# Optimization experiments

Hardware: AMD Instinct MI355X
Metric: run time of the kernel (lower is better)

Reference implementation:

```python
import jax, jax.numpy as jnp
import numpy as np

N, K, P, A, NBINS, RP = 4096, 48, 128, 5, 16, 32
LN_EPS = 1e-5

def _normalize(v, eps=1e-6):
    return v / jnp.sqrt(jnp.maximum((v * v).sum(-1, keepdims=True), eps))

def extract_frames(pos):
    # pos: [N, A, 3]; atom order N, CA, C, ... -> Gram-Schmidt backbone frame
    n, ca, c = pos[:, 0], pos[:, 1], pos[:, 2]
    e1 = _normalize(c - ca)
    v2 = n - ca
    e2 = _normalize(v2 - (v2 * e1).sum(-1, keepdims=True) * e1)
    e3 = jnp.cross(e1, e2)
    R = jnp.stack([e1, e2, e3], axis=-1)  # [N,3,3], columns = frame axes
    return R, ca

def distance_rbf(d, d_min=0.0, d_max=22.0, bins=NBINS):
    step = (d_max - d_min) / bins
    centers = d_min + step * jnp.arange(bins, dtype=d.dtype)
    return jnp.exp(-(((d[..., None] - centers) / step) ** 2))

def relpos_features(resi, chain, batch, neighbours):
    # clipped relative sequence position, extra class for cross-chain/batch pairs
    rel = jnp.clip(resi[neighbours] - resi[:, None], -RP, RP) + RP
    same = (chain[neighbours] == chain[:, None]) & (batch[neighbours] == batch[:, None])
    cls = jnp.where(same, rel, 2 * RP + 1)
    return jax.nn.one_hot(cls, 2 * RP + 2, dtype=jnp.float32)  # [N,K,66]

def distance_features(pos, neighbours):
    pn = pos[neighbours]  # [N,K,A,3] gather
    diff = pos[:, None, :, None] - pn[:, :, None, :]  # [N,K,A,A,3]
    d = jnp.sqrt(jnp.maximum((diff * diff).sum(-1), 1e-12))
    return distance_rbf(d).reshape(N, K, A * A * NBINS)

def direction_features(pos, neighbours, R, ca):
    rel = pos[neighbours] - ca[:, None, None]  # [N,K,A,3]
    local = jnp.einsum('nji,nkaj->nkai', R, rel)  # express in frame of residue i
    return _normalize(local).reshape(N, K, A * 3)

def rotation_features(neighbours, R):
    Rrel = jnp.einsum('nji,nkjl->nkil', R, R[neighbours])  # R_i^T R_j
    return Rrel.reshape(N, K, 9)

def pair_vector_features(pos, neighbours, R, ca):
    rel = pos[neighbours] - ca[:, None, None]
    local = jnp.einsum('nji,nkaj->nkai', R, rel)
    return local.reshape(N, K, A * 3)

def setup_inputs() -> dict:
    key = jax.random.key(0)
    ks = jax.random.split(key, 12)
    s = 0.02
    pos = 5.0 * jax.random.normal(ks[0], (N, A, 3), dtype=jnp.float32)
    dmap = 22.0 * jax.random.uniform(ks[1], (N, N), dtype=jnp.float32)
    mask = jnp.ones((N,), dtype=jnp.float32)
    neighbours = jax.random.randint(ks[2], (N, K), 0, N, dtype=jnp.int32)
    resi = jnp.arange(N, dtype=jnp.int32)
    chain = jnp.zeros((N,), dtype=jnp.int32)
    batch = jnp.zeros((N,), dtype=jnp.int32)
    W_relpos = s * jax.random.normal(ks[3], (2 * RP + 2, P), dtype=jnp.float32)
    W_dmap = s * jax.random.normal(ks[4], (NBINS, P), dtype=jnp.float32)
    W_dist = s * jax.random.normal(ks[5], (A * A * NBINS, P), dtype=jnp.float32)
    W_dir = s * jax.random.normal(ks[6], (3 * A, P), dtype=jnp.float32)
    W_rot = s * jax.random.normal(ks[7], (9, P), dtype=jnp.float32)
    W_vec = s * jax.random.normal(ks[8], (3 * A, P), dtype=jnp.float32)
    ln_scale = jnp.ones((P,), dtype=jnp.float32)
    ln_offset = jnp.zeros((P,), dtype=jnp.float32)
    W1 = s * jax.random.normal(ks[9], (P, 2 * P), dtype=jnp.float32)
    b1 = jnp.zeros((2 * P,), dtype=jnp.float32)
    W2 = s * jax.random.normal(ks[10], (2 * P, P), dtype=jnp.float32)
    b2 = jnp.zeros((P,), dtype=jnp.float32)
    return dict(pos=pos, dmap=dmap, mask=mask, W_relpos=W_relpos, W_dmap=W_dmap,
                W_dist=W_dist, W_dir=W_dir, W_rot=W_rot, W_vec=W_vec,
                ln_scale=ln_scale, ln_offset=ln_offset, W1=W1, b1=b1, W2=W2, b2=b2,
                neighbours=neighbours, resi=resi, chain=chain, batch=batch)

def reference(pos, dmap, mask, W_relpos, W_dmap, W_dist, W_dir, W_rot, W_vec,
              ln_scale, ln_offset, W1, b1, W2, b2, neighbours, resi, chain, batch):
    pair_mask = mask[:, None] * mask[neighbours] * (neighbours != -1).astype(mask.dtype)
    R, ca = extract_frames(pos)
    idx = jnp.arange(N)
    dmap_nb = dmap[idx[:, None], neighbours]  # [N,K] gather of distance map
    # multi-branch linear sum
    pair = relpos_features(resi, chain, batch, neighbours) @ W_relpos
    pair += jnp.where(pair_mask[..., None] > 0, distance_rbf(dmap_nb), 0.0) @ W_dmap
    pair += distance_features(pos, neighbours) @ W_dist
    pair += direction_features(pos, neighbours, R, ca) @ W_dir
    pair += rotation_features(neighbours, R) @ W_rot
    pair += pair_vector_features(pos, neighbours, R, ca) @ W_vec
    # LayerNorm (create_scale=True, create_offset=True)
    mu = pair.mean(-1, keepdims=True)
    var = ((pair - mu) ** 2).mean(-1, keepdims=True)
    pair = (pair - mu) / jnp.sqrt(var + LN_EPS) * ln_scale + ln_offset
    # MLP(2P -> P) with gelu
    pair = jax.nn.gelu(pair @ W1 + b1) @ W2 + b2
    return pair, pair_mask
```

## Files before the change

### kernel.cpp

```cpp
#include <hip/hip_runtime.h>
#include <hip/hip_bf16.h>

#define N_RES 4096
#define KNB   48
#define PCH   128
#define INV_STEP 0.727272727272727f
#define E2INV 0.13533528323661270f

typedef __bf16 bf16x8 __attribute__((ext_vector_type(8)));
typedef float  f32x4  __attribute__((ext_vector_type(4)));

#define FOCT(o,m) (((o)*49 + (m))*8)

__device__ __align__(16) unsigned short g_wcat[60*128*8];
__device__ __align__(16) unsigned short g_w1[16*256*8];
__device__ __align__(16) unsigned short g_w2[32*128*8];

__device__ __forceinline__ unsigned short f2bf(float f) {
  unsigned int u = __float_as_uint(f);
  return (unsigned short)((u + 0x7fffu + ((u >> 16) & 1u)) >> 16);
}
__device__ __forceinline__ unsigned int pk2(float a, float b) {
  __hip_bfloat162 h = __float22bfloat162_rn(make_float2(a, b));
  unsigned int u; __builtin_memcpy(&u, &h, 4); return u;
}
__device__ __forceinline__ float gelu_f(float x) {
  float p = x * x;
  float q = fmaf(p, 0.044715f, 1.0f);
  float r = x * q;
  float e = __expf(-1.5957691216057308f * r);
  return x * __builtin_amdgcn_rcpf(1.0f + e);
}
__device__ __forceinline__ void frame_from_pos(const float* p, float* R) {
  float cax = p[3], cay = p[4], caz = p[5];
  float e1x = p[6]-cax, e1y = p[7]-cay, e1z = p[8]-caz;
  float i1 = __builtin_amdgcn_rsqf(fmaxf(e1x*e1x + e1y*e1y + e1z*e1z, 1e-6f));
  e1x *= i1; e1y *= i1; e1z *= i1;
  float vx = p[0]-cax, vy = p[1]-cay, vz = p[2]-caz;
  float dp = vx*e1x + vy*e1y + vz*e1z;
  float e2x = vx - dp*e1x, e2y = vy - dp*e1y, e2z = vz - dp*e1z;
  float i2 = __builtin_amdgcn_rsqf(fmaxf(e2x*e2x + e2y*e2y + e2z*e2z, 1e-6f));
  e2x *= i2; e2y *= i2; e2z *= i2;
  float e3x = e1y*e2z - e1z*e2y;
  float e3y = e1z*e2x - e1x*e2z;
  float e3z = e1x*e2y - e1y*e2x;
  R[0]=e1x; R[1]=e2x; R[2]=e3x;
  R[3]=e1y; R[4]=e2y; R[5]=e3y;
  R[6]=e1z; R[7]=e2z; R[8]=e3z;
}

__device__ __forceinline__ void stage_bins(unsigned short* sF, const float* s_xall,
                                           int xbase, int ntasks, int t) {
  for (int i = t; i < ntasks; i += 256) {
    int rloc = i / 48;
    int m = i - 48*rloc;
    float x = fminf(s_xall[(xbase + rloc)*48 + m], 25.0f);
    float u  = __expf(-x*x);
    float wu = __expf(2.0f*x - 1.0f);
    float xm = x - 15.0f;
    float d  = __expf(-xm*xm);
    float wd = __expf(-2.0f*xm - 1.0f);
    float bins[16];
    bins[0] = u;
    #pragma unroll
    for (int b = 1; b < 16; ++b) { u *= wu; wu *= E2INV; bins[b] = u; }
    bins[15] = fmaxf(bins[15], d);
    #pragma unroll
    for (int b = 14; b >= 0; --b) { d *= wd; wd *= E2INV; bins[b] = fmaxf(bins[b], d); }
    unsigned int p0 = pk2(bins[0], bins[1]),  p1 = pk2(bins[2], bins[3]);
    unsigned int p2 = pk2(bins[4], bins[5]),  p3 = pk2(bins[6], bins[7]);
    unsigned int p4 = pk2(bins[8], bins[9]),  p5 = pk2(bins[10], bins[11]);
    unsigned int p6 = pk2(bins[12], bins[13]),p7 = pk2(bins[14], bins[15]);
    int base = FOCT(2*rloc, m);
    *(uint4*)(sF + base)       = make_uint4(p0,p1,p2,p3);
    *(uint4*)(sF + base + 392) = make_uint4(p4,p5,p6,p7);
  }
}

__global__ __launch_bounds__(256) void prep_weights(
    const float* __restrict__ W_dmap, const float* __restrict__ W_dist,
    const float* __restrict__ W_dir, const float* __restrict__ W_rot,
    const float* __restrict__ W_vec, const float* __restrict__ W1,
    const float* __restrict__ W2)
{
  int i = blockIdx.x*256 + threadIdx.x;
  unsigned short pk[8];
  if (i < 7680) {
    int oct = i >> 7, col = i & 127;
    #pragma unroll
    for (int j = 0; j < 8; ++j) {
      int k = oct*8 + j;
      float v;
      if      (k < 16)  v = W_dmap[k*128 + col];
      else if (k < 416) v = W_dist[(k-16)*128 + col];
      else if (k < 456) {
        int a = (k-416) >> 3, jj = (k-416) & 7;
        v = (jj < 3) ? W_dir[(a*3+jj)*128 + col]
          : (jj < 6) ? W_vec[(a*3+jj-3)*128 + col] : 0.0f;
      }
      else if (k < 465) v = W_rot[(k-456)*128 + col];
      else              v = 0.0f;
      pk[j] = f2bf(v);
    }
    *(uint4*)(g_wcat + i*8) = *(uint4*)pk;
  } else if (i < 11776) {
    int j2 = i - 7680;
    int oct = j2 >> 8, col = j2 & 255;
    #pragma unroll
    for (int j = 0; j < 8; ++j) {
      int k = oct*8 + j;
      int h = 32*(k>>5) + (k&1)*16 + ((k&31)>>1);
      pk[j] = f2bf(W1[h*256 + col]);
    }
    *(uint4*)(g_w1 + j2*8) = *(uint4*)pk;
  } else if (i < 15872) {
    int j3 = i - 11776;
    int oct = j3 >> 7, col = j3 & 127;
    #pragma unroll
    for (int j = 0; j < 8; ++j) {
      int k = oct*8 + j;
      int kh = k & 127;
      int h = (k>>7)*128 + 32*(kh>>5) + (kh&1)*16 + ((kh&31)>>1);
      pk[j] = f2bf(W2[h*128 + col]);
    }
    *(uint4*)(g_w2 + j3*8) = *(uint4*)pk;
  }
}

#define MFMA6(A0,A1,A2,B0,B1,ACC) \
  ACC[0][0] = __builtin_amdgcn_mfma_f32_16x16x32_bf16(A0, B0, ACC[0][0], 0,0,0); \
  ACC[1][0] = __builtin_amdgcn_mfma_f32_16x16x32_bf16(A1, B0, ACC[1][0], 0,0,0); \
  ACC[2][0] = __builtin_amdgcn_mfma_f32_16x16x32_bf16(A2, B0, ACC[2][0], 0,0,0); \
  ACC[0][1] = __builtin_amdgcn_mfma_f32_16x16x32_bf16(A0, B1, ACC[0][1], 0,0,0); \
  ACC[1][1] = __builtin_amdgcn_mfma_f32_16x16x32_bf16(A1, B1, ACC[1][1], 0,0,0); \
  ACC[2][1] = __builtin_amdgcn_mfma_f32_16x16x32_bf16(A2, B1, ACC[2][1], 0,0,0);

__global__ __launch_bounds__(256, 6) void fused_struct_kernel(
    const float* __restrict__ pos, const float* __restrict__ dmap,
    const float* __restrict__ mask, const float* __restrict__ W_relpos,
    const float* __restrict__ ln_scale, const float* __restrict__ ln_offset,
    const float* __restrict__ b1, const float* __restrict__ b2,
    const int* __restrict__ neighbours, const int* __restrict__ resi,
    const int* __restrict__ chain, const int* __restrict__ batch,
    float* __restrict__ out)
{
  const int n = blockIdx.x;
  const int t = threadIdx.x;
  const int lane = t & 63;
  const int wv   = t >> 6;
  const int ln15 = lane & 15;
  const int quad = lane >> 4;

  __shared__ __align__(16) char regF[12544];
  __shared__ __align__(16) char regP[12544];
  __shared__ __align__(16) float2 s_stats[48];

  unsigned short* sF    = (unsigned short*)regF;
  unsigned short* sPair = (unsigned short*)regP;
  float*  s_posnb = (float*)regP;
  float*  s_Rnb   = (float*)(regP + 3264);
  float*  s_xall  = (float*)(regP + 5760);
  float*  s_posn  = (float*)(regP + 10752);
  float*  s_Rn    = (float*)(regP + 10816);
  int*    s_cls   = (int*)  (regP + 10880);
  float2* s_part  = (float2*)(regP + 11072);

  if (t < KNB) {
    const int k = t;
    const int nbraw = neighbours[n*KNB + k];
    int nb = nbraw; if (nb < 0) nb += N_RES;
    float p[15];
    const float* pp = pos + nb*15;
    #pragma unroll
    for (int d = 0; d < 15; ++d) { p[d] = pp[d]; s_posnb[k*17+d] = p[d]; }
    float R[9];
    frame_from_pos(p, R);
    #pragma unroll
    for (int d = 0; d < 9; ++d) s_Rnb[k*13+d] = R[d];

    float pm = mask[n] * mask[nb] * ((nbraw != -1) ? 1.0f : 0.0f);
    out[N_RES*KNB*PCH + n*KNB + k] = pm;

    int rel = resi[nb] - resi[n];
    rel = (rel < -32) ? -32 : (rel > 32 ? 32 : rel);
    rel += 32;
    bool same = (chain[nb] == chain[n]) && (batch[nb] == batch[n]);
    s_cls[k] = same ? rel : 65;

    float xd = dmap[(long long)n*N_RES + nb] * INV_STEP;
    s_xall[k] = (pm > 0.0f) ? xd : 30.0f;
  } else if (t == 255) {
    float p[15];
    const float* pp = pos + n*15;
    #pragma unroll
    for (int d = 0; d < 15; ++d) { p[d] = pp[d]; s_posn[d] = p[d]; }
    float R[9];
    frame_from_pos(p, R);
    #pragma unroll
    for (int d = 0; d < 9; ++d) s_Rn[d] = R[d];
  }
  __syncthreads();

  for (int idx = t; idx < 1200; idx += 256) {
    int c = idx / 48, k = idx - 48*c;
    int a1 = c / 5, a2 = c - 5*a1;
    float dx = s_posn[a1*3+0] - s_posnb[k*17 + a2*3+0];
    float dy = s_posn[a1*3+1] - s_posnb[k*17 + a2*3+1];
    float dz = s_posn[a1*3+2] - s_posnb[k*17 + a2*3+2];
    float d2 = dx*dx + dy*dy + dz*dz;
    s_xall[48 + idx] = sqrtf(fmaxf(d2, 1e-12f)) * INV_STEP;
  }

  float rp0[12], rp1[12];
  {
    int c0 = 32*wv + ln15;
    #pragma unroll
    for (int mt = 0; mt < 3; ++mt)
      #pragma unroll
      for (int r = 0; r < 4; ++r) {
        int row = mt*16 + quad*4 + r;
        const float* wr = W_relpos + s_cls[row]*128 + c0;
        rp0[mt*4+r] = wr[0];
        rp1[mt*4+r] = wr[16];
      }
  }
  __syncthreads();

  f32x4 acc1[3][2] = {};

  #pragma unroll 1
  for (int st = 0; st < 3; ++st) {
    stage_bins(sF, s_xall, st*8, 384, t);
    __syncthreads();
    #pragma unroll
    for (int kc = 0; kc < 4; ++kc) {
      const unsigned short* ab = sF + FOCT(kc*4 + quad, ln15);
      bf16x8 a0 = *(const bf16x8*)(ab);
      bf16x8 a1 = *(const bf16x8*)(ab + 128);
      bf16x8 a2 = *(const bf16x8*)(ab + 256);
      const unsigned short* bb = g_wcat + (((st*4+kc)*4 + quad)*128 + 32*wv + ln15)*8;
      bf16x8 b0 = *(const bf16x8*)(bb);
      bf16x8 b1v= *(const bf16x8*)(bb + 128);
      MFMA6(a0,a1,a2,b0,b1v,acc1)
    }
    __syncthreads();
  }

  stage_bins(sF, s_xall, 24, 96, t);
  if (t < 240) {
    int k = t / 5, a = t - 5*k;
    float rx = s_posnb[k*17 + a*3+0] - s_posn[3];
    float ry = s_posnb[k*17 + a*3+1] - s_posn[4];
    float rz = s_posnb[k*17 + a*3+2] - s_posn[5];
    float l0 = s_Rn[0]*rx + s_Rn[3]*ry + s_Rn[6]*rz;
    float l1 = s_Rn[1]*rx + s_Rn[4]*ry + s_Rn[7]*rz;
    float l2 = s_Rn[2]*rx + s_Rn[5]*ry + s_Rn[8]*rz;
    float inv = __builtin_amdgcn_rsqf(fmaxf(l0*l0 + l1*l1 + l2*l2, 1e-6f));
    *(uint4*)(sF + FOCT(4+a, k)) =
        make_uint4(pk2(l0*inv, l1*inv), pk2(l2*inv, l0), pk2(l1, l2), 0u);
  }
  if (t >= 208) {
    int k = t - 208;
    float rr[9];
    #pragma unroll
    for (int il = 0; il < 9; ++il) {
      int i2 = il / 3, l2c = il - 3*i2;
      rr[il] = s_Rn[0+i2]*s_Rnb[k*13 + 0+l2c]
             + s_Rn[3+i2]*s_Rnb[k*13 + 3+l2c]
             + s_Rn[6+i2]*s_Rnb[k*13 + 6+l2c];
    }
    *(uint4*)(sF + FOCT(9, k))  = make_uint4(pk2(rr[0],rr[1]), pk2(rr[2],rr[3]),
                                             pk2(rr[4],rr[5]), pk2(rr[6],rr[7]));
    *(uint4*)(sF + FOCT(10, k)) = make_uint4(pk2(rr[8],0.0f), 0u, 0u, 0u);
    *(uint4*)(sF + FOCT(11, k)) = make_uint4(0u, 0u, 0u, 0u);
  }
  __syncthreads();
  #pragma unroll
  for (int kc = 0; kc < 3; ++kc) {
    const unsigned short* ab = sF + FOCT(kc*4 + quad, ln15);
    bf16x8 a0 = *(const bf16x8*)(ab);
    bf16x8 a1 = *(const bf16x8*)(ab + 128);
    bf16x8 a2 = *(const bf16x8*)(ab + 256);
    const unsigned short* bb = g_wcat + (((12+kc)*4 + quad)*128 + 32*wv + ln15)*8;
    bf16x8 b0 = *(const bf16x8*)(bb);
    bf16x8 b1v= *(const bf16x8*)(bb + 128);
    MFMA6(a0,a1,a2,b0,b1v,acc1)
  }

  #pragma unroll
  for (int mt = 0; mt < 3; ++mt)
    #pragma unroll
    for (int r = 0; r < 4; ++r) {
      acc1[mt][0][r] += rp0[mt*4+r];
      acc1[mt][1][r] += rp1[mt*4+r];
    }

  #pragma unroll
  for (int mt = 0; mt < 3; ++mt)
    #pragma unroll
    for (int r = 0; r < 4; ++r) {
      float a0v = acc1[mt][0][r], a1v = acc1[mt][1][r];
      float sv = a0v + a1v;
      float qv = a0v*a0v + a1v*a1v;
      #pragma unroll
      for (int msk = 1; msk < 16; msk <<= 1) {
        sv += __shfl_xor(sv, msk);
        qv += __shfl_xor(qv, msk);
      }
      if (ln15 == 0) s_part[wv*48 + mt*16 + quad*4 + r] = make_float2(sv, qv);
    }
  __syncthreads();
  if (t < 48) {
    float S = 0.0f, Q = 0.0f;
    #pragma unroll
    for (int w = 0; w < 4; ++w) { float2 p = s_part[w*48 + t]; S += p.x; Q += p.y; }
    float mu = S * (1.0f/128.0f);
    float var = Q * (1.0f/128.0f) - mu*mu;
    s_stats[t] = make_float2(mu, __builtin_amdgcn_rsqf(var + 1e-5f));
  }
  __syncthreads();
  {
    int c0 = 32*wv + ln15;
    float gg0 = ln_scale[c0],  gg1 = ln_scale[c0+16];
    float oo0 = ln_offset[c0], oo1 = ln_offset[c0+16];
    int kp = 32*wv + 2*ln15;
    int oct = kp >> 3, slot = kp & 7;
    #pragma unroll
    for (int mt = 0; mt < 3; ++mt)
      #pragma unroll
      for (int r = 0; r < 4; ++r) {
        int row = mt*16 + quad*4 + r;
        float2 stt = s_stats[row];
        float v0 = (acc1[mt][0][r] - stt.x)*stt.y*gg0 + oo0;
        float v1 = (acc1[mt][1][r] - stt.x)*stt.y*gg1 + oo1;
        *(unsigned int*)(sPair + FOCT(oct,row) + slot) = pk2(v0, v1);
      }
  }
  __syncthreads();

  f32x4 acc3[3][2] = {};
  #pragma unroll 1
  for (int half = 0; half < 2; ++half) {
    f32x4 acc2[3][2] = {};
    #pragma unroll
    for (int kc = 0; kc < 4; ++kc) {
      const unsigned short* ab = sPair + FOCT(kc*4 + quad, ln15);
      bf16x8 a0 = *(const bf16x8*)(ab);
      bf16x8 a1 = *(const bf16x8*)(ab + 128);
      bf16x8 a2 = *(const bf16x8*)(ab + 256);
      const unsigned short* bb = g_w1 + ((kc*4 + quad)*256 + half*128 + 32*wv + ln15)*8;
      bf16x8 b0 = *(const bf16x8*)(bb);
      bf16x8 b1v= *(const bf16x8*)(bb + 128);
      MFMA6(a0,a1,a2,b0,b1v,acc2)
    }
    __syncthreads();
    {
      int hc = half*128 + 32*wv + ln15;
      float bb0 = b1[hc], bb1 = b1[hc+16];
      int kp = 32*wv + 2*ln15;
      int oct = kp >> 3, slot = kp & 7;
      #pragma unroll
      for (int mt = 0; mt < 3; ++mt)
        #pragma unroll
        for (int r = 0; r < 4; ++r) {
          int row = mt*16 + quad*4 + r;
          float h0 = gelu_f(acc2[mt][0][r] + bb0);
          float h1 = gelu_f(acc2[mt][1][r] + bb1);
          *(unsigned int*)(sF + FOCT(oct,row) + slot) = pk2(h0, h1);
        }
    }
    __syncthreads();
    #pragma unroll
    for (int kc = 0; kc < 4; ++kc) {
      const unsigned short* ab = sF + FOCT(kc*4 + quad, ln15);
      bf16x8 a0 = *(const bf16x8*)(ab);
      bf16x8 a1 = *(const bf16x8*)(ab + 128);
      bf16x8 a2 = *(const bf16x8*)(ab + 256);
      const unsigned short* bb = g_w2 + (((half*4 + kc)*4 + quad)*128 + 32*wv + ln15)*8;
      bf16x8 b0 = *(const bf16x8*)(bb);
      bf16x8 b1v= *(const bf16x8*)(bb + 128);
      MFMA6(a0,a1,a2,b0,b1v,acc3)
    }
  }

  {
    int c0 = 32*wv + ln15;
    float bo0 = b2[c0], bo1 = b2[c0+16];
    #pragma unroll
    for (int mt = 0; mt < 3; ++mt)
      #pragma unroll
      for (int r = 0; r < 4; ++r) {
        int row = mt*16 + quad*4 + r;
        out[(n*KNB + row)*PCH + c0]      = acc3[mt][0][r] + bo0;
        out[(n*KNB + row)*PCH + c0 + 16] = acc3[mt][1][r] + bo1;
      }
  }
}

extern "C" void kernel_launch(void* const* d_in, const int* in_sizes, int n_in,
                              void* d_out, int out_size, void* d_ws, size_t ws_size,
                              hipStream_t stream) {
  const float* pos       = (const float*)d_in[0];
  const float* dmap      = (const float*)d_in[1];
  const float* mask      = (const float*)d_in[2];
  const float* W_relpos  = (const float*)d_in[3];
  const float* W_dmap    = (const float*)d_in[4];
  const float* W_dist    = (const float*)d_in[5];
  const float* W_dir     = (const float*)d_in[6];
  const float* W_rot     = (const float*)d_in[7];
  const float* W_vec     = (const float*)d_in[8];
  const float* ln_scale  = (const float*)d_in[9];
  const float* ln_offset = (const float*)d_in[10];
  const float* W1        = (const float*)d_in[11];
  const float* b1        = (const float*)d_in[12];
  const float* W2        = (const float*)d_in[13];
  const float* b2        = (const float*)d_in[14];
  const int* neighbours  = (const int*)d_in[15];
  const int* resi        = (const int*)d_in[16];
  const int* chain       = (const int*)d_in[17];
  const int* batch       = (const int*)d_in[18];
  float* out = (float*)d_out;

  hipLaunchKernelGGL(prep_weights, dim3(62), dim3(256), 0, stream,
                     W_dmap, W_dist, W_dir, W_rot, W_vec, W1, W2);
  hipLaunchKernelGGL(fused_struct_kernel, dim3(N_RES), dim3(256), 0, stream,
                     pos, dmap, mask, W_relpos, ln_scale, ln_offset, b1, b2,
                     neighbours, resi, chain, batch, out);
}
```

Measured before the change: 293.7 us.

## Compute both MLP hidden halves at once and defer relpos weight gather

The two-pass loop over the MLP hidden dimension is replaced by one pass that computes all 256 hidden columns together. The GELU output goes to two shared buffers (sF and the reused pair buffer), and the second matmul then runs as a single 8-chunk loop. This removes two barriers and the serialized half loop, and lets more MFMAs issue back to back. The relpos weight gather now happens after the first GEMM instead of being held in 24 registers across it. The price is more live accumulator registers, which could raise register pressure or cause spills under launch_bounds(256,6), and the regP buffer grows slightly.

```diff
diff --git a/kernel.cpp b/kernel.cpp
--- a/kernel.cpp
+++ b/kernel.cpp
@@ -152,7 +152,7 @@
   const int quad = lane >> 4;
 
   __shared__ __align__(16) char regF[12544];
-  __shared__ __align__(16) char regP[12544];
+  __shared__ __align__(16) char regP[12672];
   __shared__ __align__(16) float2 s_stats[48];
 
   unsigned short* sF    = (unsigned short*)regF;
@@ -209,20 +209,6 @@
     float dz = s_posn[a1*3+2] - s_posnb[k*17 + a2*3+2];
     float d2 = dx*dx + dy*dy + dz*dz;
     s_xall[48 + idx] = sqrtf(fmaxf(d2, 1e-12f)) * INV_STEP;
-  }
-
-  float rp0[12], rp1[12];
-  {
-    int c0 = 32*wv + ln15;
-    #pragma unroll
-    for (int mt = 0; mt < 3; ++mt)
-      #pragma unroll
-      for (int r = 0; r < 4; ++r) {
-        int row = mt*16 + quad*4 + r;
-        const float* wr = W_relpos + s_cls[row]*128 + c0;
-        rp0[mt*4+r] = wr[0];
-        rp1[mt*4+r] = wr[16];
-      }
   }
   __syncthreads();
 
@@ -287,13 +273,18 @@
     MFMA6(a0,a1,a2,b0,b1v,acc1)
   }
 
-  #pragma unroll
-  for (int mt = 0; mt < 3; ++mt)
-    #pragma unroll
-    for (int r = 0; r < 4; ++r) {
-      acc1[mt][0][r] += rp0[mt*4+r];
-      acc1[mt][1][r] += rp1[mt*4+r];
-    }
+  {
+    int c0 = 32*wv + ln15;
+    #pragma unroll
+    for (int mt = 0; mt < 3; ++mt)
+      #pragma unroll
+      for (int r = 0; r < 4; ++r) {
+        int row = mt*16 + quad*4 + r;
+        const float* wr = W_relpos + s_cls[row]*128 + c0;
+        acc1[mt][0][r] += wr[0];
+        acc1[mt][1][r] += wr[16];
+      }
+  }
 
   #pragma unroll
   for (int mt = 0; mt < 3; ++mt)
@@ -338,49 +329,53 @@
   }
   __syncthreads();
 
+  f32x4 acc2a[3][2] = {};
+  f32x4 acc2b[3][2] = {};
+  #pragma unroll
+  for (int kc = 0; kc < 4; ++kc) {
+    const unsigned short* ab = sPair + FOCT(kc*4 + quad, ln15);
+    bf16x8 a0 = *(const bf16x8*)(ab);
+    bf16x8 a1 = *(const bf16x8*)(ab + 128);
+    bf16x8 a2 = *(const bf16x8*)(ab + 256);
+    const unsigned short* bb = g_w1 + ((kc*4 + quad)*256 + 32*wv + ln15)*8;
+    bf16x8 b0 = *(const bf16x8*)(bb);
+    bf16x8 b1v= *(const bf16x8*)(bb + 128);
+    bf16x8 b2v= *(const bf16x8*)(bb + 1024);
+    bf16x8 b3v= *(const bf16x8*)(bb + 1152);
+    MFMA6(a0,a1,a2,b0,b1v,acc2a)
+    MFMA6(a0,a1,a2,b2v,b3v,acc2b)
+  }
+  __syncthreads();
+  {
+    int hc = 32*wv + ln15;
+    float bb0 = b1[hc],     bb1 = b1[hc+16];
+    float bb2 = b1[hc+128], bb3 = b1[hc+144];
+    int kp = 32*wv + 2*ln15;
+    int oct = kp >> 3, slot = kp & 7;
+    #pragma unroll
+    for (int mt = 0; mt < 3; ++mt)
+      #pragma unroll
+      for (int r = 0; r < 4; ++r) {
+        int row = mt*16 + quad*4 + r;
+        *(unsigned int*)(sF + FOCT(oct,row) + slot) =
+            pk2(gelu_f(acc2a[mt][0][r] + bb0), gelu_f(acc2a[mt][1][r] + bb1));
+        *(unsigned int*)(sPair + FOCT(oct,row) + slot) =
+            pk2(gelu_f(acc2b[mt][0][r] + bb2), gelu_f(acc2b[mt][1][r] + bb3));
+      }
+  }
+  __syncthreads();
   f32x4 acc3[3][2] = {};
-  #pragma unroll 1
-  for (int half = 0; half < 2; ++half) {
-    f32x4 acc2[3][2] = {};
-    #pragma unroll
-    for (int kc = 0; kc < 4; ++kc) {
-      const unsigned short* ab = sPair + FOCT(kc*4 + quad, ln15);
-      bf16x8 a0 = *(const bf16x8*)(ab);
-      bf16x8 a1 = *(const bf16x8*)(ab + 128);
-      bf16x8 a2 = *(const bf16x8*)(ab + 256);
-      const unsigned short* bb = g_w1 + ((kc*4 + quad)*256 + half*128 + 32*wv + ln15)*8;
-      bf16x8 b0 = *(const bf16x8*)(bb);
-      bf16x8 b1v= *(const bf16x8*)(bb + 128);
-      MFMA6(a0,a1,a2,b0,b1v,acc2)
-    }
-    __syncthreads();
-    {
-      int hc = half*128 + 32*wv + ln15;
-      float bb0 = b1[hc], bb1 = b1[hc+16];
-      int kp = 32*wv + 2*ln15;
-      int oct = kp >> 3, slot = kp & 7;
-      #pragma unroll
-      for (int mt = 0; mt < 3; ++mt)
-        #pragma unroll
-        for (int r = 0; r < 4; ++r) {
-          int row = mt*16 + quad*4 + r;
-          float h0 = gelu_f(acc2[mt][0][r] + bb0);
-          float h1 = gelu_f(acc2[mt][1][r] + bb1);
-          *(unsigned int*)(sF + FOCT(oct,row) + slot) = pk2(h0, h1);
-        }
-    }
-    __syncthreads();
-    #pragma unroll
-    for (int kc = 0; kc < 4; ++kc) {
-      const unsigned short* ab = sF + FOCT(kc*4 + quad, ln15);
-      bf16x8 a0 = *(const bf16x8*)(ab);
-      bf16x8 a1 = *(const bf16x8*)(ab + 128);
-      bf16x8 a2 = *(const bf16x8*)(ab + 256);
-      const unsigned short* bb = g_w2 + (((half*4 + kc)*4 + quad)*128 + 32*wv + ln15)*8;
-      bf16x8 b0 = *(const bf16x8*)(bb);
-      bf16x8 b1v= *(const bf16x8*)(bb + 128);
-      MFMA6(a0,a1,a2,b0,b1v,acc3)
-    }
+  #pragma unroll
+  for (int kc2 = 0; kc2 < 8; ++kc2) {
+    const unsigned short* src = (kc2 < 4) ? sF : sPair;
+    const unsigned short* ab = src + FOCT((kc2 & 3)*4 + quad, ln15);
+    bf16x8 a0 = *(const bf16x8*)(ab);
+    bf16x8 a1 = *(const bf16x8*)(ab + 128);
+    bf16x8 a2 = *(const bf16x8*)(ab + 256);
+    const unsigned short* bb = g_w2 + ((kc2*4 + quad)*128 + 32*wv + ln15)*8;
+    bf16x8 b0 = *(const bf16x8*)(bb);
+    bf16x8 b1v= *(const bf16x8*)(bb + 128);
+    MFMA6(a0,a1,a2,b0,b1v,acc3)
   }
 
   {
```

Result: faster. 274.9 us (-6.4%).
